# Performance work log

Measured on AMD Instinct MI355X. Metric: run time of the kernel, lower is better.

Reference implementation:

```python
import jax, jax.numpy as jnp
import numpy as np
from jax.scipy.linalg import solve_triangular

N_SAMPLES = 8192
N_STEPS = 200
DX, DU, DY, DB = 8, 4, 8, 128
SIGMA_Y = 0.1  # observation noise std of the Gaussian likelihood


def setup_inputs() -> dict:
    key = jax.random.key(0)
    ks = jax.random.split(key, 9)
    observations = jax.random.normal(ks[0], (N_STEPS, DY), dtype=jnp.float32)
    inputs = jax.random.normal(ks[1], (N_STEPS, DU), dtype=jnp.float32)
    init_state_mean = jnp.zeros((DX,), dtype=jnp.float32)
    A = jax.random.normal(ks[2], (DX, DX), dtype=jnp.float32) * 0.1
    init_state_cov = A @ A.T + 0.5 * jnp.eye(DX, dtype=jnp.float32)
    coeff_mat = jax.random.normal(ks[3], (DX, DB), dtype=jnp.float32) * 0.05
    B = jax.random.normal(ks[4], (DX, DX), dtype=jnp.float32) * 0.1
    error_cov = B @ B.T + 0.05 * jnp.eye(DX, dtype=jnp.float32)
    ref_state = jax.random.normal(ks[5], (N_STEPS, DX), dtype=jnp.float32)
    Omega = jax.random.normal(ks[6], (DB, DX + DU), dtype=jnp.float32)
    phase = jax.random.uniform(ks[7], (DB,), dtype=jnp.float32, maxval=2.0 * np.pi)
    C = jax.random.normal(ks[8], (DY, DX), dtype=jnp.float32) * 0.3
    return dict(observations=observations, inputs=inputs,
                init_state_mean=init_state_mean, init_state_cov=init_state_cov,
                coeff_mat=coeff_mat, error_cov=error_cov, ref_state=ref_state,
                Omega=Omega, phase=phase, C=C, seed=0)


def _basis_all(state, u_t, Omega, phase):
    # state: [N, DX], u_t: [DU] -> random Fourier features [N, DB]
    z = jnp.concatenate([state, jnp.broadcast_to(u_t, (state.shape[0], u_t.shape[0]))], axis=1)
    return jnp.cos(z @ Omega.T + phase)


def _loglik(y, x_batch, C):
    # Gaussian log N(y; C x, SIGMA_Y^2 I) for each particle: [N]
    r = y - x_batch @ C.T
    dy = y.shape[0]
    return (-0.5 * jnp.sum(r * r, axis=-1) / (SIGMA_Y * SIGMA_Y)
            - 0.5 * dy * jnp.log(jnp.asarray(2.0 * np.pi * SIGMA_Y * SIGMA_Y, r.dtype)))


def _mvn_logpdf_shared_cov(x, means, L):
    # log N(x; means[i], L L^T) for each row of means: [N]
    diff = x - means  # [N, DX]
    sol = solve_triangular(L, diff.T, lower=True)  # [DX, N]
    dx = x.shape[0]
    return (-0.5 * jnp.sum(sol * sol, axis=0)
            - jnp.sum(jnp.log(jnp.diag(L)))
            - 0.5 * dx * jnp.log(jnp.asarray(2.0 * np.pi, x.dtype)))


def _systematic_sisr(key, weights):
    # systematic resampling: stratified positions against the weight CDF
    n = weights.shape[0]
    u = jax.random.uniform(key, dtype=weights.dtype)
    positions = (jnp.arange(n, dtype=weights.dtype) + u) / n
    return jnp.searchsorted(jnp.cumsum(weights), positions)


def _csmc_forward(observations, inputs, init_state_mean, init_state_cov,
                  coeff_mat, error_cov, ref_state, Omega, phase, C, seed):
    key = jax.random.key(seed)
    key, key_init = jax.random.split(key)
    L0 = jnp.linalg.cholesky(init_state_cov)
    L_err = jnp.linalg.cholesky(error_cov)

    # init particles ~ MVN(mean, cov); last particle pinned to reference
    eps0 = jax.random.normal(key_init, (N_SAMPLES, DX), dtype=init_state_mean.dtype)
    state0 = init_state_mean + eps0 @ L0.T
    state0 = state0.at[-1].set(ref_state[0])
    log_w0 = jnp.zeros((N_SAMPLES,), dtype=state0.dtype)

    def scan_step(carry, xs):
        key, log_w, state = carry
        obs_t, inp_t, ref_t = xs
        key, key_step = jax.random.split(key)

        basis = _basis_all(state, inp_t, Omega, phase)          # [N, DB]
        aux_state = basis @ coeff_mat.T                         # [N, DX] (== propagation mean)
        ll_aux = _loglik(obs_t, aux_state, C)                   # [N]
        log_w_aux = ll_aux + log_w
        aux_weights = jax.nn.softmax(log_w_aux)

        key_step, k_anc = jax.random.split(key_step)
        a_idx = _systematic_sisr(k_anc, aux_weights)            # [N]

        h_x = _mvn_logpdf_shared_cov(ref_t, aux_state, L_err)
        w_anc = jax.nn.softmax(log_w_aux + h_x)
        key_step, k_ref = jax.random.split(key_step)
        ref_idx = jnp.searchsorted(jnp.cumsum(w_anc), jax.random.uniform(k_ref, dtype=w_anc.dtype))
        a_idx = a_idx.at[-1].set(ref_idx)

        key_step, k_state = jax.random.split(key_step)
        eps = jax.random.normal(k_state, (N_SAMPLES, DX), dtype=state.dtype)
        new_state = aux_state + eps @ L_err.T                   # MVN(mean, error_cov)
        new_state = new_state.at[-1].set(ref_t)

        new_log_w = _loglik(obs_t, new_state, C) - ll_aux[a_idx]
        return (key, new_log_w, new_state), (new_state, new_log_w, a_idx)

    xs = (observations[1:], inputs[1:], ref_state[1:])
    (key, log_w_last, _), (states, log_ws, ancestors) = jax.lax.scan(
        scan_step, (key, log_w0, state0), xs)

    state_trace = jnp.concatenate([state0[None], states], axis=0)  # [T, N, DX]

    # sample final index, then backtrack ancestors to reconstruct one trajectory
    w = jax.nn.softmax(log_w_last)
    idx = jnp.searchsorted(jnp.cumsum(w), jax.random.uniform(key, dtype=w.dtype))

    def back_step(b_t, anc_row):
        return anc_row[b_t], b_t
    b0, bs = jax.lax.scan(back_step, idx, ancestors, reverse=True)
    idx_all = jnp.concatenate([b0[None], bs])                   # [T]
    return state_trace[jnp.arange(N_STEPS), idx_all]            # [T, DX]


def reference(observations, inputs, init_state_mean, init_state_cov,
              coeff_mat, error_cov, ref_state, Omega, phase, C, seed):
    return _csmc_forward(observations, inputs, init_state_mean, init_state_cov,
                         coeff_mat, error_cov, ref_state, Omega, phase, C, seed)
```

## Files before the change

kernel.cpp:

```cpp
#include <hip/hip_runtime.h>
#include <stdint.h>
#include <math.h>

#define NS 8192
#define NSTEPS 200
#define DBc 128

typedef unsigned int u32;
typedef unsigned short u16;

#define WS_KEYINIT 64
#define WS_KFIN   66
#define WS_KC     128
#define WS_KST    640
#define WS_IDX    2048
#define WS_U1     2560
#define WS_U2     2816
#define WS_LL     4096
#define WS_H      (WS_LL+NSTEPS*NS)
#define WS_LLN    (WS_H+NSTEPS*NS)
#define WS_ANC_F  (WS_LLN+NSTEPS*NS)
#define WS_CKPT   (WS_ANC_F+(NSTEPS-1)*NS/2)

__device__ __forceinline__ u32 rotl32(u32 v, int r){ return (v<<r)|(v>>(32-r)); }

__device__ __forceinline__ void tf2x32(u32 k0,u32 k1,u32 c0,u32 c1,u32&o0,u32&o1){
  u32 ks2 = k0^k1^0x1BD11BDAu;
  u32 x0=c0+k0, x1=c1+k1;
#define TFR(R) { x0+=x1; x1=rotl32(x1,(R)); x1^=x0; }
  TFR(13) TFR(15) TFR(26) TFR(6)
  x0+=k1;  x1+=ks2+1u;
  TFR(17) TFR(29) TFR(16) TFR(24)
  x0+=ks2; x1+=k0+2u;
  TFR(13) TFR(15) TFR(26) TFR(6)
  x0+=k0;  x1+=k1+3u;
  TFR(17) TFR(29) TFR(16) TFR(24)
  x0+=k1;  x1+=ks2+4u;
  TFR(13) TFR(15) TFR(26) TFR(6)
  x0+=ks2; x1+=k0+5u;
#undef TFR
  o0=x0; o1=x1;
}

__device__ __forceinline__ u32 jax_bits_elem(u32 k0,u32 k1,u32 i){
  u32 a,b; tf2x32(k0,k1,0u,i,a,b); return a^b;
}

__device__ __forceinline__ float bits_to_f01(u32 bits){
  return __uint_as_float((bits>>9)|0x3f800000u) - 1.0f;
}

__device__ __forceinline__ float log1pf_acc(float a){
#pragma clang fp contract(off)
  float u = 1.0f + a;
  if (u == 1.0f) return a;
  float l = logf(u);
  return l * (a / (u - 1.0f));
}

__device__ __forceinline__ float erfinv_xla(float x){
#pragma clang fp contract(off)
  float a = -(x*x);
  float w = -log1pf_acc(a);
  float p;
  if (w < 5.0f){
    w = w - 2.5f;
    p = 2.81022636e-08f;
    p = 3.43273939e-07f + p*w;
    p = -3.5233877e-06f + p*w;
    p = -4.39150654e-06f + p*w;
    p = 0.00021858087f  + p*w;
    p = -0.00125372503f + p*w;
    p = -0.00417768164f + p*w;
    p = 0.246640727f    + p*w;
    p = 1.50140941f     + p*w;
  } else {
    w = sqrtf(w) - 3.0f;
    p = -0.000200214257f;
    p = 0.000100950558f + p*w;
    p = 0.00134934322f  + p*w;
    p = -0.00367342844f + p*w;
    p = 0.00573950773f  + p*w;
    p = -0.0076224613f  + p*w;
    p = 0.00943887047f  + p*w;
    p = 1.00167406f     + p*w;
    p = 2.83297682f     + p*w;
  }
  return p*x;
}

__device__ __forceinline__ float jax_normal_elem(u32 k0,u32 k1,u32 i){
#pragma clang fp contract(off)
  float f = bits_to_f01(jax_bits_elem(k0,k1,i));
  float u = f*2.0f + (-0.99999994039535522f);
  u = fmaxf(-0.99999994039535522f, u);
  return 1.41421356237309515f * erfinv_xla(u);
}

__device__ __forceinline__ float jax_uniform01_scalar(u32 k0,u32 k1){
  return bits_to_f01(jax_bits_elem(k0,k1,0u));
}

__device__ __forceinline__ float wave_max(float v){
  #pragma unroll
  for(int m=1;m<64;m<<=1) v=fmaxf(v,__shfl_xor(v,m,64));
  return v;
}
__device__ __forceinline__ float wave_incl_scan(float v,int lane){
  #pragma unroll
  for(int o=1;o<64;o<<=1){ float u=__shfl_up(v,o,64); if(lane>=o) v+=u; }
  return v;
}

__device__ void chol8(const float* A,float* L){
  for(int c=0;c<8;c++){
    for(int r=c;r<8;r++){
      float s=A[r*8+c];
      for(int k=0;k<c;k++) s-=L[r*(r+1)/2+k]*L[c*(c+1)/2+k];
      L[r*(r+1)/2+c]=(r==c)? sqrtf(s) : s/L[c*(c+1)/2+c];
    }
  }
}

__device__ __forceinline__ int srch_from(const float* C,float tau,int lo0,int guess){
  int lo=lo0, hi=NS;
  int p=guess; if(p>NS-1)p=NS-1; if(p<lo0)p=lo0;
  if(C[p]>=tau){
    hi=p+1;
    int off=1;
    while(true){
      int q=p-off;
      if(q<lo0) break;
      if(C[q]>=tau){ hi=q+1; off<<=1; }
      else { lo=q+1; break; }
    }
  } else {
    lo=p+1;
    int off=1;
    while(true){
      int q=p+off;
      if(q>NS-1) break;
      if(C[q]<tau){ lo=q+1; off<<=1; }
      else { hi=q+1; break; }
    }
  }
  while(lo<hi){ int mid=(lo+hi)>>1; if(C[mid]<tau) lo=mid+1; else hi=mid; }
  return lo;
}

__global__ __launch_bounds__(256) void k_pre(const int* __restrict__ seedp, float* wsf){
  u32* KI=(u32*)(wsf+WS_KEYINIT); u32* KF=(u32*)(wsf+WS_KFIN);
  u32* KC=(u32*)(wsf+WS_KC); u32* KST=(u32*)(wsf+WS_KST);
  int tid=threadIdx.x;
  if(tid==0){
    u32 s=(u32)seedp[0];
    u32 a,b;
    tf2x32(0u,s,0u,0u,a,b); KC[0]=a; KC[1]=b;
    tf2x32(0u,s,0u,1u,a,b); KI[0]=a; KI[1]=b;
    for(int t=1;t<NSTEPS;t++){
      tf2x32(KC[2*(t-1)],KC[2*(t-1)+1],0u,0u,a,b);
      KC[2*t]=a; KC[2*t+1]=b;
    }
    KF[0]=KC[2*(NSTEPS-1)]; KF[1]=KC[2*(NSTEPS-1)+1];
  }
  __syncthreads();
  int t=tid;
  if(t>=1 && t<NSTEPS){
    u32 k0=KC[2*(t-1)], k1=KC[2*(t-1)+1];
    u32 s0,s1; tf2x32(k0,k1,0u,1u,s0,s1);
    u32 ka0,ka1; tf2x32(s0,s1,0u,1u,ka0,ka1);
    u32 t0,t1;  tf2x32(s0,s1,0u,0u,t0,t1);
    u32 kr0,kr1; tf2x32(t0,t1,0u,1u,kr0,kr1);
    u32 u0,u1;  tf2x32(t0,t1,0u,0u,u0,u1);
    u32 w0,w1;  tf2x32(u0,u1,0u,1u,w0,w1);
    u32* p=KST+6*(t-1);
    p[0]=ka0;p[1]=ka1;p[2]=kr0;p[3]=kr1;p[4]=w0;p[5]=w1;
    wsf[WS_U1+t]=bits_to_f01(jax_bits_elem(ka0,ka1,0u));
    wsf[WS_U2+t]=bits_to_f01(jax_bits_elem(kr0,kr1,0u));
  }
}

__global__ __launch_bounds__(320,1) void k_state(
    const float* __restrict__ obs, const float* __restrict__ inp,
    const float* __restrict__ mean, const float* __restrict__ icov,
    const float* __restrict__ coeff, const float* __restrict__ ecov,
    const float* __restrict__ refst, const float* __restrict__ Om,
    const float* __restrict__ ph, const float* __restrict__ Cm,
    float* wsf)
{
  __shared__ float s_Om[DBc*12];
  __shared__ float s_cfT[DBc*8];
  __shared__ float s_ph[DBc];
  __shared__ float s_Cm[64];
  __shared__ float s_obs[NSTEPS*8];
  __shared__ float s_ref[NSTEPS*8];
  __shared__ float s_inp[NSTEPS*4];
  __shared__ u32   s_k[(NSTEPS-1)*2];
  __shared__ float s_st[64*9];
  __shared__ float s_b[64*129];

  const int tid=threadIdx.x;
  for(int x=tid;x<DBc*12;x+=320) s_Om[x]=Om[x];
  for(int x=tid;x<DBc*8;x+=320){ int j=x>>3,d=x&7; s_cfT[x]=coeff[d*DBc+j]; }
  for(int x=tid;x<DBc;x+=320) s_ph[x]=ph[x];
  for(int x=tid;x<64;x+=320) s_Cm[x]=Cm[x];
  for(int x=tid;x<NSTEPS*8;x+=320) s_obs[x]=obs[x];
  for(int x=tid;x<NSTEPS*8;x+=320) s_ref[x]=refst[x];
  for(int x=tid;x<NSTEPS*4;x+=320) s_inp[x]=inp[x];
  { const u32* KST=(const u32*)(wsf+WS_KST);
    for(int x=tid;x<(NSTEPS-1)*2;x+=320){ int tt=x>>1; s_k[x]=KST[6*tt+4+(x&1)]; } }
  __syncthreads();

  const float4* s_Om4=(const float4*)s_Om;
  const float4* s_cf4=(const float4*)s_cfT;

  if(tid<64){
    const int i=blockIdx.x*64+tid;
    const u32* KI=(const u32*)(wsf+WS_KEYINIT);
    float* LL=wsf+WS_LL; float* H=wsf+WS_H; float* LLN=wsf+WS_LLN;
    float* CKPT=wsf+WS_CKPT;

    float LEp[36];
    float L0p[36];
    chol8(icov,L0p); chol8(ecov,LEp);
    float st[8];
    if(i==NS-1){ for(int d=0;d<8;d++) st[d]=s_ref[d]; }
    else {
      float eps[8];
      #pragma unroll
      for(int d=0;d<8;d++) eps[d]=jax_normal_elem(KI[0],KI[1],(u32)(i*8+d));
      for(int d=0;d<8;d++){ float m=0.0f; for(int k=0;k<=d;k++) m+=eps[k]*L0p[d*(d+1)/2+k]; st[d]=mean[d]+m; }
    }
    { float* ck=CKPT+(size_t)i*8;
      for(int d=0;d<8;d++) ck[d]=st[d]; }

    float c_ll=4.0f*logf((float)(2.0*M_PI*0.1*0.1));
    float hc1=0.0f; for(int d=0;d<8;d++) hc1+=logf(LEp[d*(d+1)/2+d]);
    float hc2=4.0f*logf((float)(2.0*M_PI));
    const float SSQ=(float)(0.1*0.1);

    for(int t=1;t<NSTEPS;t++){
      #pragma unroll
      for(int d=0;d<8;d++) s_st[tid*9+d]=st[d];
      __syncthreads();
      __syncthreads();

      float ax[8]={0,0,0,0,0,0,0,0};
      for(int j=0;j<DBc;j++){
        float b=s_b[tid*129+j];
        float4 c0=s_cf4[j*2+0],c1=s_cf4[j*2+1];
        ax[0]+=b*c0.x; ax[1]+=b*c0.y; ax[2]+=b*c0.z; ax[3]+=b*c0.w;
        ax[4]+=b*c1.x; ax[5]+=b*c1.y; ax[6]+=b*c1.z; ax[7]+=b*c1.w;
      }
      float S=0.0f;
      for(int d=0;d<8;d++){
        float m=0.0f;
        #pragma unroll
        for(int k=0;k<8;k++) m+=ax[k]*s_Cm[d*8+k];
        float r=s_obs[t*8+d]-m; S+=r*r;
      }
      float ll=(-0.5f*S)/SSQ - c_ll;
      float sol[8]; float q=0.0f;
      for(int d=0;d<8;d++){
        float s=s_ref[t*8+d]-ax[d];
        for(int k=0;k<d;k++) s-=LEp[d*(d+1)/2+k]*sol[k];
        sol[d]=s/LEp[d*(d+1)/2+d];
        q+=sol[d]*sol[d];
      }
      float h=(-0.5f*q - hc1) - hc2;
      LL[(size_t)t*NS+i]=ll;
      H[(size_t)t*NS+i]=h;

      if(i==NS-1){ for(int d=0;d<8;d++) st[d]=s_ref[t*8+d]; }
      else {
        const u32 kp4=s_k[2*(t-1)], kp5=s_k[2*(t-1)+1];
        float eps[8];
        #pragma unroll
        for(int d=0;d<8;d++) eps[d]=jax_normal_elem(kp4,kp5,(u32)(i*8+d));
        for(int d=0;d<8;d++){ float m=0.0f; for(int k=0;k<=d;k++) m+=eps[k]*LEp[d*(d+1)/2+k]; st[d]=ax[d]+m; }
      }
      float S2n=0.0f;
      for(int d=0;d<8;d++){
        float m=0.0f;
        #pragma unroll
        for(int k=0;k<8;k++) m+=st[k]*s_Cm[d*8+k];
        float r=s_obs[t*8+d]-m; S2n+=r*r;
      }
      float lln=(-0.5f*S2n)/SSQ - c_ll;
      LLN[(size_t)t*NS+i]=lln;

      if((t&7)==0){
        float* ck=CKPT+((size_t)(t>>3)*NS+i)*8;
        for(int d=0;d<8;d++) ck[d]=st[d];
      }
    }
  } else {
    const int l=tid-64;
    const int p=l&63;
    const int jg=l>>6;
    for(int t=1;t<NSTEPS;t++){
      __syncthreads();
      float z[12];
      #pragma unroll
      for(int d=0;d<8;d++) z[d]=s_st[p*9+d];
      z[8]=s_inp[t*4+0]; z[9]=s_inp[t*4+1]; z[10]=s_inp[t*4+2]; z[11]=s_inp[t*4+3];
      for(int jj=0;jj<32;jj++){
        const int j=jg*32+jj;
        float4 o0=s_Om4[j*3+0],o1=s_Om4[j*3+1],o2=s_Om4[j*3+2];
        float dot=0.0f;
        dot+=z[0]*o0.x; dot+=z[1]*o0.y; dot+=z[2]*o0.z; dot+=z[3]*o0.w;
        dot+=z[4]*o1.x; dot+=z[5]*o1.y; dot+=z[6]*o1.z; dot+=z[7]*o1.w;
        dot+=z[8]*o2.x; dot+=z[9]*o2.y; dot+=z[10]*o2.z; dot+=z[11]*o2.w;
        float dd=dot+s_ph[j];
        s_b[p*129+j]=cosf(dd);
      }
      __syncthreads();
    }
  }
}

__global__ __launch_bounds__(1024) void k_weights(float* wsf){
  const int tid=threadIdx.x;
  const int lane=tid&63;
  const int wid=tid>>6;
  const int base=tid*8;
  const u32* KF=(const u32*)(wsf+WS_KFIN);
  const float* LL=wsf+WS_LL;
  const float* H=wsf+WS_H;
  const float* LLN=wsf+WS_LLN;
  u16* ANC=(u16*)(wsf+WS_ANC_F);
  int* IDX=(int*)(wsf+WS_IDX);

  __shared__ float CUM[NS];
  __shared__ float CUM2[NS];
  __shared__ float LLS[NS];
  __shared__ float WMX[16],WMX2[16],WSM[16],WSM2[16];
  __shared__ float s_U1[NSTEPS], s_U2[NSTEPS];

  for(int x=tid;x<NSTEPS;x+=1024){ s_U1[x]=wsf[WS_U1+x]; s_U2[x]=wsf[WS_U2+x]; }

  float lw[8];
  #pragma unroll
  for(int k=0;k<8;k++) lw[k]=0.0f;

  float r_ll[8],r_h[8],r_lln[8];
  {
    const float* LLt=LL+(size_t)1*NS;
    const float* Ht=H+(size_t)1*NS;
    const float* LLNt=LLN+(size_t)1*NS;
    #pragma unroll
    for(int k=0;k<8;k++){ r_ll[k]=LLt[base+k]; r_h[k]=Ht[base+k]; r_lln[k]=LLNt[base+k]; }
  }

  for(int t=1;t<NSTEPS;t++){
    float s1v[8],s2v[8];
    float m1=-INFINITY,m2=-INFINITY;
    #pragma unroll
    for(int k=0;k<8;k++){
      float llv=r_ll[k], hv=r_h[k];
      s1v[k]=llv+lw[k];
      s2v[k]=s1v[k]+hv;
      m1=fmaxf(m1,s1v[k]); m2=fmaxf(m2,s2v[k]);
    }
    float wm1=wave_max(m1), wm2=wave_max(m2);
    if(lane==0){ WMX[wid]=wm1; WMX2[wid]=wm2; }
    __syncthreads();
    #pragma unroll
    for(int k=0;k<8;k++) LLS[base+k]=r_ll[k];
    float M1=WMX[0],M2=WMX2[0];
    #pragma unroll
    for(int w=1;w<16;w++){ M1=fmaxf(M1,WMX[w]); M2=fmaxf(M2,WMX2[w]); }

    float e1[8],e2[8]; float ts1=0.0f,ts2=0.0f;
    #pragma unroll
    for(int k=0;k<8;k++){
      e1[k]=expf(s1v[k]-M1); ts1+=e1[k];
      e2[k]=expf(s2v[k]-M2); ts2+=e2[k];
    }
    float is1=wave_incl_scan(ts1,lane);
    float is2=wave_incl_scan(ts2,lane);
    if(lane==63){ WSM[wid]=is1; WSM2[wid]=is2; }
    __syncthreads();
    float T1=0.0f,T2=0.0f,woff1=0.0f,woff2=0.0f;
    #pragma unroll
    for(int w=0;w<16;w++){
      float a=WSM[w], b=WSM2[w];
      T1+=a; T2+=b;
      if(w<wid){ woff1+=a; woff2+=b; }
    }
    float excl1=woff1+(is1-ts1);
    float excl2=woff2+(is2-ts2);

    { float run=excl1;
      #pragma unroll
      for(int k=0;k<8;k++){ run+=e1[k]; CUM[base+k]=run; } }
    { float run=excl2;
      #pragma unroll
      for(int k=0;k<8;k++){ run+=e2[k]; CUM2[base+k]=run; } }
    __syncthreads();

    float cur_lln[8];
    #pragma unroll
    for(int k=0;k<8;k++) cur_lln[k]=r_lln[k];
    if(t+1<NSTEPS){
      const float* LLt2=LL+(size_t)(t+1)*NS;
      const float* Ht2=H+(size_t)(t+1)*NS;
      const float* LLNt2=LLN+(size_t)(t+1)*NS;
      #pragma unroll
      for(int k=0;k<8;k++){ r_ll[k]=LLt2[base+k]; r_h[k]=Ht2[base+k]; r_lln[k]=LLNt2[base+k]; }
    }

    float lwn[8];
    float u1=s_U1[t];
    int prev=0;
    #pragma unroll
    for(int k=0;k<8;k++){
      int i=base+k;
      if(i!=NS-1){
        float pos=((float)i+u1)*(1.0f/8192.0f);
        float tau=pos*T1;
        int lo=(k==0)? srch_from(CUM,tau,0,i)
                     : srch_from(CUM,tau,prev,prev);
        if(lo>NS-1) lo=NS-1;
        prev=lo;
        ANC[(size_t)(t-1)*NS+i]=(u16)lo;
        lwn[k]=cur_lln[k]-LLS[lo];
      }
    }
    if(tid==1023){
      float u2=s_U2[t];
      float tau=u2*T2;
      int lo=0,hi=NS;
      while(lo<hi){ int mid=(lo+hi)>>1; if(CUM2[mid]<tau) lo=mid+1; else hi=mid; }
      if(lo>NS-1) lo=NS-1;
      ANC[(size_t)(t-1)*NS+(NS-1)]=(u16)lo;
      lwn[7]=cur_lln[7]-LLS[lo];
    }
    #pragma unroll
    for(int k=0;k<8;k++) lw[k]=lwn[k];
  }

  {
    float m=-INFINITY;
    #pragma unroll
    for(int k=0;k<8;k++) m=fmaxf(m,lw[k]);
    float wm=wave_max(m);
    if(lane==0) WMX[wid]=wm;
    __syncthreads();
    float M=WMX[0];
    #pragma unroll
    for(int w=1;w<16;w++) M=fmaxf(M,WMX[w]);
    float e[8]; float ts=0.0f;
    #pragma unroll
    for(int k=0;k<8;k++){ e[k]=expf(lw[k]-M); ts+=e[k]; }
    float is=wave_incl_scan(ts,lane);
    if(lane==63) WSM[wid]=is;
    __syncthreads();
    float T=0.0f,woff=0.0f;
    #pragma unroll
    for(int w=0;w<16;w++){ T+=WSM[w]; if(w<wid) woff+=WSM[w]; }
    float run=woff+(is-ts);
    #pragma unroll
    for(int k=0;k<8;k++){ run+=e[k]; CUM[base+k]=run; }
    __syncthreads();
    if(tid==0){
      float u=jax_uniform01_scalar(KF[0],KF[1]);
      float tau=u*T;
      int lo=0,hi=NS;
      while(lo<hi){ int mid=(lo+hi)>>1; if(CUM[mid]<tau) lo=mid+1; else hi=mid; }
      if(lo>NS-1) lo=NS-1;
      int b=lo;
      IDX[NSTEPS-1]=b;
      for(int r=NSTEPS-2;r>=0;r--){ b=(int)ANC[(size_t)r*NS+b]; IDX[r]=b; }
    }
  }
}

__global__ __launch_bounds__(256) void k_replay(
    const float* __restrict__ inp, const float* __restrict__ refst,
    const float* __restrict__ ecov, const float* __restrict__ Om,
    const float* __restrict__ ph, const float* __restrict__ coeff,
    const float* __restrict__ wsf, float* __restrict__ out)
{
  int task=blockIdx.x*blockDim.x+threadIdx.x;
  if(task>=NSTEPS) return;
  const int* IDX=(const int*)(wsf+WS_IDX);
  const u32* KST=(const u32*)(wsf+WS_KST);
  const float* CKPT=wsf+WS_CKPT;
  int t=task, p=IDX[t];
  if(p==NS-1){ for(int d=0;d<8;d++) out[t*8+d]=refst[t*8+d]; return; }
  float LEp[36]; chol8(ecov,LEp);
  int c=(t>>3)<<3;
  const float* ck=CKPT+((size_t)(t>>3)*NS+p)*8;
  float st[8];
  for(int d=0;d<8;d++) st[d]=ck[d];
  for(int s=c+1;s<=t;s++){
    float z[12];
    for(int d=0;d<8;d++) z[d]=st[d];
    for(int k=0;k<4;k++) z[8+k]=inp[s*4+k];
    float ax[8]={0,0,0,0,0,0,0,0};
    #pragma unroll 2
    for(int j=0;j<DBc;j++){
      float dot=0.0f;
      #pragma unroll
      for(int k=0;k<12;k++) dot+=z[k]*Om[j*12+k];
      float b=cosf(dot+ph[j]);
      #pragma unroll
      for(int d=0;d<8;d++) ax[d]+=b*coeff[d*DBc+j];
    }
    const u32* kp=KST+6*(s-1);
    float eps[8];
    #pragma unroll
    for(int d=0;d<8;d++) eps[d]=jax_normal_elem(kp[4],kp[5],(u32)(p*8+d));
    for(int d=0;d<8;d++){ float m=0.0f; for(int k=0;k<=d;k++) m+=eps[k]*LEp[d*(d+1)/2+k]; st[d]=ax[d]+m; }
  }
  for(int d=0;d<8;d++) out[t*8+d]=st[d];
}

extern "C" void kernel_launch(void* const* d_in, const int* in_sizes, int n_in,
                              void* d_out, int out_size, void* d_ws, size_t ws_size,
                              hipStream_t stream) {
  const float* obs  =(const float*)d_in[0];
  const float* inp  =(const float*)d_in[1];
  const float* mean =(const float*)d_in[2];
  const float* icov =(const float*)d_in[3];
  const float* coeff=(const float*)d_in[4];
  const float* ecov =(const float*)d_in[5];
  const float* refst=(const float*)d_in[6];
  const float* Om   =(const float*)d_in[7];
  const float* ph   =(const float*)d_in[8];
  const float* Cm   =(const float*)d_in[9];
  const int*   seedp=(const int*)d_in[10];
  float* wsf=(float*)d_ws;
  float* out=(float*)d_out;

  hipLaunchKernelGGL(k_pre, dim3(1), dim3(256), 0, stream, seedp, wsf);
  hipLaunchKernelGGL(k_state, dim3(NS/64), dim3(320), 0, stream,
                     obs, inp, mean, icov, coeff, ecov, refst, Om, ph, Cm, wsf);
  hipLaunchKernelGGL(k_weights, dim3(1), dim3(1024), 0, stream, wsf);
  hipLaunchKernelGGL(k_replay, dim3(1), dim3(256), 0, stream,
                     inp, refst, ecov, Om, ph, coeff, wsf, out);
}
```

Measured before the change: 4.664 ms.

## Invert systematic resampling search into per-source scatter of ancestor indices

Rather than having each particle search the cumulative weight array for its ancestor, each source particle now finds the range of stratified positions its cumulative weight covers, using a binary search over the closed-form position formula. It then scatters its own index into a shared SLO table for that range. After a barrier, each particle reads its ancestor from the table. This removes the data-dependent galloping searches over shared memory, at the cost of an extra barrier, a new shared array, and write loops whose length varies with particle weight.

After: 8.745 ms. 1.88x slower.

```diff
diff --git a/kernel.cpp b/kernel.cpp
--- a/kernel.cpp
+++ b/kernel.cpp
@@ -122,30 +122,15 @@
   }
 }
 
-__device__ __forceinline__ int srch_from(const float* C,float tau,int lo0,int guess){
-  int lo=lo0, hi=NS;
-  int p=guess; if(p>NS-1)p=NS-1; if(p<lo0)p=lo0;
-  if(C[p]>=tau){
-    hi=p+1;
-    int off=1;
-    while(true){
-      int q=p-off;
-      if(q<lo0) break;
-      if(C[q]>=tau){ hi=q+1; off<<=1; }
-      else { lo=q+1; break; }
-    }
-  } else {
-    lo=p+1;
-    int off=1;
-    while(true){
-      int q=p+off;
-      if(q>NS-1) break;
-      if(C[q]<tau){ lo=q+1; off<<=1; }
-      else { hi=q+1; break; }
-    }
-  }
-  while(lo<hi){ int mid=(lo+hi)>>1; if(C[mid]<tau) lo=mid+1; else hi=mid; }
-  return lo;
+__device__ __forceinline__ int h_of(float Cm, float u1, float T1){
+  int lo=0, hi=NS;
+  while(lo<hi){
+    int mid=(lo+hi)>>1;
+    float pos=((float)mid+u1)*(1.0f/8192.0f);
+    float tau=pos*T1;
+    if(tau<=Cm) lo=mid+1; else hi=mid;
+  }
+  return lo-1;
 }
 
 __global__ __launch_bounds__(256) void k_pre(const int* __restrict__ seedp, float* wsf){
@@ -334,6 +319,7 @@
   __shared__ float CUM[NS];
   __shared__ float CUM2[NS];
   __shared__ float LLS[NS];
+  __shared__ u16   SLO[NS];
   __shared__ float WMX[16],WMX2[16],WSM[16],WSM2[16];
   __shared__ float s_U1[NSTEPS], s_U2[NSTEPS];
 
@@ -391,9 +377,10 @@
     float excl1=woff1+(is1-ts1);
     float excl2=woff2+(is2-ts2);
 
+    float runv[8];
     { float run=excl1;
       #pragma unroll
-      for(int k=0;k<8;k++){ run+=e1[k]; CUM[base+k]=run; } }
+      for(int k=0;k<8;k++){ run+=e1[k]; CUM[base+k]=run; runv[k]=run; } }
     { float run=excl2;
       #pragma unroll
       for(int k=0;k<8;k++){ run+=e2[k]; CUM2[base+k]=run; } }
@@ -410,23 +397,21 @@
       for(int k=0;k<8;k++){ r_ll[k]=LLt2[base+k]; r_h[k]=Ht2[base+k]; r_lln[k]=LLNt2[base+k]; }
     }
 
+    float u1=s_U1[t];
+    int hm[8];
+    #pragma unroll
+    for(int k=0;k<8;k++) hm[k]=h_of(runv[k],u1,T1);
+    int prevh;
+    if(base==0) prevh=-1;
+    else prevh=h_of(CUM[base-1],u1,T1);
+    #pragma unroll
+    for(int k=0;k<8;k++){
+      int m=base+k;
+      int iHi=(m==NS-1)? (NS-1) : hm[k];
+      for(int i=prevh+1;i<=iHi;i++) SLO[i]=(u16)m;
+      prevh=hm[k];
+    }
     float lwn[8];
-    float u1=s_U1[t];
-    int prev=0;
-    #pragma unroll
-    for(int k=0;k<8;k++){
-      int i=base+k;
-      if(i!=NS-1){
-        float pos=((float)i+u1)*(1.0f/8192.0f);
-        float tau=pos*T1;
-        int lo=(k==0)? srch_from(CUM,tau,0,i)
-                     : srch_from(CUM,tau,prev,prev);
-        if(lo>NS-1) lo=NS-1;
-        prev=lo;
-        ANC[(size_t)(t-1)*NS+i]=(u16)lo;
-        lwn[k]=cur_lln[k]-LLS[lo];
-      }
-    }
     if(tid==1023){
       float u2=s_U2[t];
       float tau=u2*T2;
@@ -435,6 +420,17 @@
       if(lo>NS-1) lo=NS-1;
       ANC[(size_t)(t-1)*NS+(NS-1)]=(u16)lo;
       lwn[7]=cur_lln[7]-LLS[lo];
+    }
+    __syncthreads();
+
+    #pragma unroll
+    for(int k=0;k<8;k++){
+      int i=base+k;
+      if(i!=NS-1){
+        int lo=(int)SLO[i];
+        ANC[(size_t)(t-1)*NS+i]=(u16)lo;
+        lwn[k]=cur_lln[k]-LLS[lo];
+      }
     }
     #pragma unroll
     for(int k=0;k<8;k++) lw[k]=lwn[k];
```

## Parallelize trajectory replay across one wavefront per timestep with shuffle reductions

Applied to the files above, without the earlier changes.

The replay kernel previously ran one thread per timestep in a single block, with each thread looping serially over all 128 basis functions for up to 7 recomputed steps. It now launches one 64-lane wavefront per timestep, splits the basis loop across lanes, reduces with xor shuffles, and computes the 8 noise samples in parallel before broadcasting them. The Cholesky and small loops are fully unrolled so arrays can stay in registers. This shortens the serial tail at the end of the pipeline, at the cost of shuffle overhead and redundant Cholesky work in every lane.

After: 4.435 ms (median of 2 runs). 1.05x faster.

```diff
diff --git a/kernel.cpp b/kernel.cpp
--- a/kernel.cpp
+++ b/kernel.cpp
@@ -122,6 +122,21 @@
   }
 }
 
+__device__ __forceinline__ void chol8u(const float* A,float* L){
+  #pragma unroll
+  for(int c=0;c<8;c++){
+    #pragma unroll
+    for(int r=0;r<8;r++){
+      if(r>=c){
+        float s=A[r*8+c];
+        #pragma unroll
+        for(int k=0;k<8;k++) if(k<c) s-=L[r*(r+1)/2+k]*L[c*(c+1)/2+k];
+        L[r*(r+1)/2+c]=(r==c)? sqrtf(s) : s/L[c*(c+1)/2+c];
+      }
+    }
+  }
+}
+
 __device__ __forceinline__ int srch_from(const float* C,float tau,int lo0,int guess){
   int lo=lo0, hi=NS;
   int p=guess; if(p>NS-1)p=NS-1; if(p<lo0)p=lo0;
@@ -476,31 +491,40 @@
   }
 }
 
-__global__ __launch_bounds__(256) void k_replay(
+__global__ __launch_bounds__(64) void k_replay(
     const float* __restrict__ inp, const float* __restrict__ refst,
     const float* __restrict__ ecov, const float* __restrict__ Om,
     const float* __restrict__ ph, const float* __restrict__ coeff,
     const float* __restrict__ wsf, float* __restrict__ out)
 {
-  int task=blockIdx.x*blockDim.x+threadIdx.x;
-  if(task>=NSTEPS) return;
+  const int t=blockIdx.x;
+  const int lane=threadIdx.x;
   const int* IDX=(const int*)(wsf+WS_IDX);
   const u32* KST=(const u32*)(wsf+WS_KST);
   const float* CKPT=wsf+WS_CKPT;
-  int t=task, p=IDX[t];
-  if(p==NS-1){ for(int d=0;d<8;d++) out[t*8+d]=refst[t*8+d]; return; }
-  float LEp[36]; chol8(ecov,LEp);
+  int p=IDX[t];
+  if(p==NS-1){
+    if(lane<8) out[t*8+lane]=refst[t*8+lane];
+    return;
+  }
+  float LEp[36]; chol8u(ecov,LEp);
   int c=(t>>3)<<3;
   const float* ck=CKPT+((size_t)(t>>3)*NS+p)*8;
   float st[8];
+  #pragma unroll
   for(int d=0;d<8;d++) st[d]=ck[d];
   for(int s=c+1;s<=t;s++){
     float z[12];
+    #pragma unroll
     for(int d=0;d<8;d++) z[d]=st[d];
+    #pragma unroll
     for(int k=0;k<4;k++) z[8+k]=inp[s*4+k];
-    float ax[8]={0,0,0,0,0,0,0,0};
-    #pragma unroll 2
-    for(int j=0;j<DBc;j++){
+    float ax[8];
+    #pragma unroll
+    for(int d=0;d<8;d++) ax[d]=0.0f;
+    #pragma unroll
+    for(int jj=0;jj<2;jj++){
+      const int j=lane+jj*64;
       float dot=0.0f;
       #pragma unroll
       for(int k=0;k<12;k++) dot+=z[k]*Om[j*12+k];
@@ -508,13 +532,25 @@
       #pragma unroll
       for(int d=0;d<8;d++) ax[d]+=b*coeff[d*DBc+j];
     }
+    #pragma unroll
+    for(int m=1;m<64;m<<=1){
+      #pragma unroll
+      for(int d=0;d<8;d++) ax[d]+=__shfl_xor(ax[d],m,64);
+    }
     const u32* kp=KST+6*(s-1);
+    float eo=jax_normal_elem(kp[4],kp[5],(u32)(p*8+(lane&7)));
     float eps[8];
     #pragma unroll
-    for(int d=0;d<8;d++) eps[d]=jax_normal_elem(kp[4],kp[5],(u32)(p*8+d));
-    for(int d=0;d<8;d++){ float m=0.0f; for(int k=0;k<=d;k++) m+=eps[k]*LEp[d*(d+1)/2+k]; st[d]=ax[d]+m; }
-  }
-  for(int d=0;d<8;d++) out[t*8+d]=st[d];
+    for(int d=0;d<8;d++) eps[d]=__shfl(eo,d,64);
+    #pragma unroll
+    for(int d=0;d<8;d++){
+      float m=0.0f;
+      #pragma unroll
+      for(int k=0;k<8;k++) if(k<=d) m+=eps[k]*LEp[d*(d+1)/2+k];
+      st[d]=ax[d]+m;
+    }
+  }
+  if(lane<8) out[t*8+lane]=st[lane];
 }
 
 extern "C" void kernel_launch(void* const* d_in, const int* in_sizes, int n_in,
@@ -538,6 +574,6 @@
   hipLaunchKernelGGL(k_state, dim3(NS/64), dim3(320), 0, stream,
                      obs, inp, mean, icov, coeff, ecov, refst, Om, ph, Cm, wsf);
   hipLaunchKernelGGL(k_weights, dim3(1), dim3(1024), 0, stream, wsf);
-  hipLaunchKernelGGL(k_replay, dim3(1), dim3(256), 0, stream,
+  hipLaunchKernelGGL(k_replay, dim3(NSTEPS), dim3(64), 0, stream,
                      inp, refst, ecov, Om, ph, coeff, wsf, out);
 }
```
